# Kernel optimization log

Measured on AMD Instinct MI355X. Metric: run time of the kernel, lower is better.

The kernel has to match this reference:

```python
import jax, jax.numpy as jnp
import numpy as np

B, D, H, L = 16384, 512, 1024, 2


def _lstm_step_zero_state(x, W_ih, W_hh, b_ih, b_hh):
    """One PyTorch-convention LSTM cell step with h0=c0=0.

    Gate order: i, f, g, o. With h0=0 the W_hh matmul contributes nothing,
    but both biases still apply (matches cuDNN/PyTorch math exactly).
    With c0=0 the forget-gate term f*c0 vanishes.
    x: (B, in), W_ih: (4H, in), W_hh: (4H, H), biases: (4H,)
    """
    gates = x @ W_ih.T + (b_ih + b_hh)  # (B, 4H)
    i, f, g, o = jnp.split(gates, 4, axis=-1)
    i = jax.nn.sigmoid(i)
    g = jnp.tanh(g)
    o = jax.nn.sigmoid(o)
    c = i * g  # f * c0 == 0
    h = o * jnp.tanh(c)
    return h


def setup_inputs() -> dict:
    key = jax.random.key(0)
    ks = jax.random.split(key, 12)
    s = 1.0 / np.sqrt(H)  # PyTorch LSTM init scale

    def u(k, shape):
        return jax.random.uniform(k, shape, jnp.float32, -s, s)

    x = jax.random.normal(ks[0], (B, D), jnp.float32)
    return {
        "x": x,
        "W_ih0": u(ks[1], (4 * H, D)),
        "W_hh0": u(ks[2], (4 * H, H)),
        "b_ih0": u(ks[3], (4 * H,)),
        "b_hh0": u(ks[4], (4 * H,)),
        "W_ih1": u(ks[5], (4 * H, H)),
        "W_hh1": u(ks[6], (4 * H, H)),
        "b_ih1": u(ks[7], (4 * H,)),
        "b_hh1": u(ks[8], (4 * H,)),
        "W_dec": u(ks[9], (D, H)),
        "b_dec": u(ks[10], (D,)),
    }


def reference(x, W_ih0, W_hh0, b_ih0, b_hh0, W_ih1, W_hh1, b_ih1, b_hh1, W_dec, b_dec):
    # forward(): x.unsqueeze(1) -> 2-layer LSTM (zero init state, 1 step) -> decoder
    h0 = _lstm_step_zero_state(x, W_ih0, W_hh0, b_ih0, b_hh0)   # (B, H)
    h1 = _lstm_step_zero_state(h0, W_ih1, W_hh1, b_ih1, b_hh1)  # (B, H)
    return h1 @ W_dec.T + b_dec  # (B, D)
```

## Files before the change

kernel.cpp:

```cpp
#include <hip/hip_runtime.h>
#include <stdint.h>


typedef __attribute__((ext_vector_type(8))) __bf16 bf16x8;
typedef __attribute__((ext_vector_type(4))) float f32x4;

#define BM 128
#define BK 64

__device__ __forceinline__ unsigned short f2b(float f) {
    unsigned int x = __builtin_bit_cast(unsigned int, f);
    x = x + 0x7FFFu + ((x >> 16) & 1u);
    return (unsigned short)(x >> 16);
}
__device__ __forceinline__ float sigf(float x) { return 1.0f / (1.0f + __expf(-x)); }
__device__ __forceinline__ float tanh_safe(float x) {
    float a = fabsf(x);
    float e = __expf(-2.0f * a);
    float t = (1.0f - e) / (1.0f + e);
    return x < 0.0f ? -t : t;
}

__device__ __forceinline__ void cvt8(const float* __restrict__ s,
                                     unsigned short* __restrict__ d) {
    f32x4 lo = *reinterpret_cast<const f32x4*>(s);
    f32x4 hi = *reinterpret_cast<const f32x4*>(s + 4);
    __attribute__((ext_vector_type(8))) unsigned short v;
    v[0] = f2b(lo[0]); v[1] = f2b(lo[1]); v[2] = f2b(lo[2]); v[3] = f2b(lo[3]);
    v[4] = f2b(hi[0]); v[5] = f2b(hi[1]); v[6] = f2b(hi[2]); v[7] = f2b(hi[3]);
    *reinterpret_cast<__attribute__((ext_vector_type(8))) unsigned short*>(d) = v;
}

__device__ __forceinline__ void gload16(const unsigned short* g, unsigned short* l) {
    __builtin_amdgcn_global_load_lds(
        (const __attribute__((address_space(1))) void*)g,
        (__attribute__((address_space(3))) void*)l,
        16, 0, 0);
}

__device__ __forceinline__ void pack_one(const float* __restrict__ W,
                                         unsigned short* __restrict__ d,
                                         int K8, int H, int c) {
    int dstRow = c / K8, kc = c - dstRow * K8;
    int G = dstRow / 192, r = dstRow - G * 192;
    int wc = r / 96, rr = r - wc * 96;
    int n = rr >> 4, i = rr & 15;
    int hsub = n / 3, gate = n - hsub * 3;
    int goff = (gate == 0) ? 0 : (gate + 1);
    int hcol = G * 64 + wc * 32 + hsub * 16 + i;
    cvt8(W + ((size_t)(goff * H + hcol) * K8 + kc) * 8, d + (size_t)c * 8);
}

__global__ __launch_bounds__(256) void prepass(
    const float* __restrict__ x,   const float* __restrict__ W0,
    const float* __restrict__ W1,  const float* __restrict__ Wd,
    unsigned short* __restrict__ xb,  unsigned short* __restrict__ wp0,
    unsigned short* __restrict__ wp1, unsigned short* __restrict__ wdecb)
{
    const int tid = threadIdx.x;
    const int b   = blockIdx.x;
    if (b < 2048) {
        int c = b * 256 + tid;
        cvt8(x + (size_t)c * 8, xb + (size_t)c * 8);
        c += 2048 * 256;
        cvt8(x + (size_t)c * 8, xb + (size_t)c * 8);
    } else if (b < 2816) {
        pack_one(W0, wp0, 64, 1024, (b - 2048) * 256 + tid);
    } else if (b < 4352) {
        pack_one(W1, wp1, 128, 1024, (b - 2816) * 256 + tid);
    } else {
        int c = (b - 4352) * 256 + tid;
        cvt8(Wd + (size_t)c * 8, wdecb + (size_t)c * 8);
    }
}

template <int GATED>
__global__ __launch_bounds__(256, 3) void gemm_fused(
    const unsigned short* __restrict__ A,
    const unsigned short* __restrict__ Wp,
    const float* __restrict__ b0,
    const float* __restrict__ b1,
    void* __restrict__ Ov,
    int M, int K, int N, int NBX)
{
    constexpr int NFR   = GATED ? 6 : 4;
    constexpr int BROWS = GATED ? 192 : 128;
    constexpr int WCS   = GATED ? 96 : 64;
    constexpr int ONB   = GATED ? 64 : 128;
    constexpr int NBCH  = BROWS / 32;

    __shared__ __align__(16) unsigned short sA[BM * BK];
    __shared__ __align__(16) unsigned short sB[BROWS * BK];

    const int tid  = threadIdx.x;
    const int lane = tid & 63;
    const int w    = tid >> 6;
    const int wr   = w >> 1, wc = w & 1;
    const int l16  = lane & 15, hi8 = lane >> 4;

    const int cpx  = gridDim.x >> 3;
    const int orig = blockIdx.x;
    const int rid  = (orig & 7) * cpx + (orig >> 3);
    const int bx   = rid % NBX;
    const int by   = rid / NBX;
    const int row0 = by * BM;
    const int n0   = bx * ONB;

    const int r0 = tid >> 3, sl = tid & 7;
    const int ls = sl ^ (r0 & 7);
    const unsigned int strd = 32u * (unsigned)K;
    unsigned int offA = (unsigned)(row0 + r0) * (unsigned)K + ls * 8;
    unsigned int offB = (unsigned)((GATED ? bx * BROWS : n0) + r0)
                        * (unsigned)K + ls * 8;

    f32x4 acc[4][NFR];
#pragma unroll
    for (int m = 0; m < 4; ++m)
#pragma unroll
        for (int n = 0; n < NFR; ++n)
            acc[m][n] = (f32x4){0.f, 0.f, 0.f, 0.f};

    for (int k0 = 0; k0 < K; k0 += BK) {
#pragma unroll
        for (int i = 0; i < 4; ++i)
            gload16(A + offA + i * strd + k0, sA + tid * 8 + i * 2048);
#pragma unroll
        for (int i = 0; i < NBCH; ++i)
            gload16(Wp + offB + i * strd + k0, sB + tid * 8 + i * 2048);
        __syncthreads();

#pragma unroll
        for (int ks = 0; ks < 2; ++ks) {
            bf16x8 av[4], bv[NFR];
#pragma unroll
            for (int m = 0; m < 4; ++m) {
                int row = wr * 64 + m * 16 + l16;
                int ps = (ks * 4 + hi8) ^ (row & 7);
                av[m] = *reinterpret_cast<const bf16x8*>(sA + row * BK + ps * 8);
            }
#pragma unroll
            for (int n = 0; n < NFR; ++n) {
                int row = wc * WCS + n * 16 + l16;
                int ps = (ks * 4 + hi8) ^ (row & 7);
                bv[n] = *reinterpret_cast<const bf16x8*>(sB + row * BK + ps * 8);
            }
#pragma unroll
            for (int m = 0; m < 4; ++m)
#pragma unroll
                for (int n = 0; n < NFR; ++n)
                    acc[m][n] = __builtin_amdgcn_mfma_f32_16x16x32_bf16(
                        av[m], bv[n], acc[m][n], 0, 0, 0);
        }
        __syncthreads();
    }

    if constexpr (GATED) {
        unsigned short* O = (unsigned short*)Ov;
#pragma unroll
        for (int hsub = 0; hsub < 2; ++hsub) {
            const int hcol = n0 + wc * 32 + hsub * 16 + l16;
            const float bi = b0[hcol]         + b1[hcol];
            const float bg = b0[2 * N + hcol] + b1[2 * N + hcol];
            const float bo = b0[3 * N + hcol] + b1[3 * N + hcol];
#pragma unroll
            for (int m = 0; m < 4; ++m) {
                int rbase = row0 + wr * 64 + m * 16 + hi8 * 4;
#pragma unroll
                for (int q = 0; q < 4; ++q) {
                    float iv = sigf(acc[m][hsub * 3 + 0][q] + bi);
                    float gv = tanh_safe(acc[m][hsub * 3 + 1][q] + bg);
                    float ov = sigf(acc[m][hsub * 3 + 2][q] + bo);
                    float h  = ov * tanh_safe(iv * gv);
                    O[(size_t)(rbase + q) * N + hcol] = f2b(h);
                }
            }
        }
    } else {
        float* O = (float*)Ov;
#pragma unroll
        for (int n = 0; n < NFR; ++n) {
            int col = n0 + wc * WCS + n * 16 + l16;
            float bias = b0[col];
#pragma unroll
            for (int m = 0; m < 4; ++m) {
                int rbase = row0 + wr * 64 + m * 16 + hi8 * 4;
#pragma unroll
                for (int q = 0; q < 4; ++q)
                    O[(size_t)(rbase + q) * N + col] = acc[m][n][q] + bias;
            }
        }
    }
}

extern "C" void kernel_launch(void* const* d_in, const int* in_sizes, int n_in,
                              void* d_out, int out_size, void* d_ws, size_t ws_size,
                              hipStream_t stream) {
    constexpr int M = 16384, D = 512, H = 1024;

    const float* x    = (const float*)d_in[0];
    const float* Wih0 = (const float*)d_in[1];
    const float* bih0 = (const float*)d_in[3];
    const float* bhh0 = (const float*)d_in[4];
    const float* Wih1 = (const float*)d_in[5];
    const float* bih1 = (const float*)d_in[7];
    const float* bhh1 = (const float*)d_in[8];
    const float* Wdec = (const float*)d_in[9];
    const float* bdec = (const float*)d_in[10];

    const size_t szH = (size_t)M * H * 2;
    const size_t sw0 = (size_t)3 * H * D * 2;
    const size_t sw1 = (size_t)3 * H * H * 2;

    unsigned short* h0 = (unsigned short*)d_ws;
    unsigned short* h1 = (unsigned short*)((char*)d_ws + szH);
    unsigned short* xb = h1;
    unsigned short* wp0   = (unsigned short*)((char*)d_ws + 2 * szH);
    unsigned short* wp1   = (unsigned short*)((char*)wp0 + sw0);
    unsigned short* wdecb = (unsigned short*)((char*)wp1 + sw1);

    prepass<<<4608, 256, 0, stream>>>(x, Wih0, Wih1, Wdec, xb, wp0, wp1, wdecb);

    gemm_fused<1><<<dim3((H / 64) * (M / BM)), 256, 0, stream>>>(
        xb, wp0, bih0, bhh0, h0, M, D, H, H / 64);
    gemm_fused<1><<<dim3((H / 64) * (M / BM)), 256, 0, stream>>>(
        h0, wp1, bih1, bhh1, h1, M, H, H, H / 64);
    gemm_fused<0><<<dim3((D / 128) * (M / BM)), 256, 0, stream>>>(
        h1, wdecb, bdec, nullptr, (float*)d_out, M, H, D, D / 128);
}
```

Measured before the change: 210.7 us.

## Switch GEMMs to 32x32x16 MFMA tiles and make K a template parameter

Replaces the 16x16x32 bf16 MFMA fragments with 32x32x16 fragments. Each wave now holds 2xNFR 32x32 accumulators instead of 4x(2*NFR) 16x16 ones, which cuts LDS fragment reads per MFMA and raises the math done per instruction. The weight packing order and the gated and plain epilogues are rewritten to match the new accumulator row and column layout. K becomes a compile-time constant so address strides fold. The risk is higher register pressure with f32x16 accumulators and a less coalesced epilogue store pattern.

```diff
diff --git a/kernel.cpp b/kernel.cpp
--- a/kernel.cpp
+++ b/kernel.cpp
@@ -4,6 +4,7 @@
 
 typedef __attribute__((ext_vector_type(8))) __bf16 bf16x8;
 typedef __attribute__((ext_vector_type(4))) float f32x4;
+typedef __attribute__((ext_vector_type(16))) float f32x16;
 
 #define BM 128
 #define BK 64
@@ -43,11 +44,10 @@
                                          int K8, int H, int c) {
     int dstRow = c / K8, kc = c - dstRow * K8;
     int G = dstRow / 192, r = dstRow - G * 192;
-    int wc = r / 96, rr = r - wc * 96;
-    int n = rr >> 4, i = rr & 15;
-    int hsub = n / 3, gate = n - hsub * 3;
+    int wcg = r / 96, rr = r - wcg * 96;
+    int gate = rr >> 5, cc = rr & 31;
     int goff = (gate == 0) ? 0 : (gate + 1);
-    int hcol = G * 64 + wc * 32 + hsub * 16 + i;
+    int hcol = G * 64 + wcg * 32 + cc;
     cvt8(W + ((size_t)(goff * H + hcol) * K8 + kc) * 8, d + (size_t)c * 8);
 }
 
@@ -74,16 +74,16 @@
     }
 }
 
-template <int GATED>
+template <int GATED, int K>
 __global__ __launch_bounds__(256, 3) void gemm_fused(
     const unsigned short* __restrict__ A,
     const unsigned short* __restrict__ Wp,
     const float* __restrict__ b0,
     const float* __restrict__ b1,
     void* __restrict__ Ov,
-    int M, int K, int N, int NBX)
+    int M, int N, int NBX)
 {
-    constexpr int NFR   = GATED ? 6 : 4;
+    constexpr int NFR   = GATED ? 3 : 2;
     constexpr int BROWS = GATED ? 192 : 128;
     constexpr int WCS   = GATED ? 96 : 64;
     constexpr int ONB   = GATED ? 64 : 128;
@@ -96,7 +96,7 @@
     const int lane = tid & 63;
     const int w    = tid >> 6;
     const int wr   = w >> 1, wc = w & 1;
-    const int l16  = lane & 15, hi8 = lane >> 4;
+    const int l32  = lane & 31, hi2 = lane >> 5;
 
     const int cpx  = gridDim.x >> 3;
     const int orig = blockIdx.x;
@@ -108,17 +108,19 @@
 
     const int r0 = tid >> 3, sl = tid & 7;
     const int ls = sl ^ (r0 & 7);
-    const unsigned int strd = 32u * (unsigned)K;
-    unsigned int offA = (unsigned)(row0 + r0) * (unsigned)K + ls * 8;
-    unsigned int offB = (unsigned)((GATED ? bx * BROWS : n0) + r0)
-                        * (unsigned)K + ls * 8;
-
-    f32x4 acc[4][NFR];
-#pragma unroll
-    for (int m = 0; m < 4; ++m)
+    constexpr unsigned int strd = 32u * (unsigned)K;
+    const unsigned int offA = (unsigned)(row0 + r0) * (unsigned)K + ls * 8;
+    const unsigned int offB = (unsigned)((GATED ? bx * BROWS : n0) + r0)
+                              * (unsigned)K + ls * 8;
+
+    f32x16 acc[2][NFR];
+#pragma unroll
+    for (int mf = 0; mf < 2; ++mf)
 #pragma unroll
         for (int n = 0; n < NFR; ++n)
-            acc[m][n] = (f32x4){0.f, 0.f, 0.f, 0.f};
+#pragma unroll
+            for (int q = 0; q < 16; ++q)
+                acc[mf][n][q] = 0.f;
 
     for (int k0 = 0; k0 < K; k0 += BK) {
 #pragma unroll
@@ -130,63 +132,63 @@
         __syncthreads();
 
 #pragma unroll
-        for (int ks = 0; ks < 2; ++ks) {
-            bf16x8 av[4], bv[NFR];
-#pragma unroll
-            for (int m = 0; m < 4; ++m) {
-                int row = wr * 64 + m * 16 + l16;
-                int ps = (ks * 4 + hi8) ^ (row & 7);
-                av[m] = *reinterpret_cast<const bf16x8*>(sA + row * BK + ps * 8);
+        for (int kst = 0; kst < 4; ++kst) {
+            bf16x8 av[2], bv[NFR];
+#pragma unroll
+            for (int mf = 0; mf < 2; ++mf) {
+                int row = wr * 64 + mf * 32 + l32;
+                int ps = (kst * 2 + hi2) ^ (row & 7);
+                av[mf] = *reinterpret_cast<const bf16x8*>(sA + row * BK + ps * 8);
             }
 #pragma unroll
             for (int n = 0; n < NFR; ++n) {
-                int row = wc * WCS + n * 16 + l16;
-                int ps = (ks * 4 + hi8) ^ (row & 7);
+                int row = wc * WCS + n * 32 + l32;
+                int ps = (kst * 2 + hi2) ^ (row & 7);
                 bv[n] = *reinterpret_cast<const bf16x8*>(sB + row * BK + ps * 8);
             }
 #pragma unroll
-            for (int m = 0; m < 4; ++m)
+            for (int mf = 0; mf < 2; ++mf)
 #pragma unroll
                 for (int n = 0; n < NFR; ++n)
-                    acc[m][n] = __builtin_amdgcn_mfma_f32_16x16x32_bf16(
-                        av[m], bv[n], acc[m][n], 0, 0, 0);
+                    acc[mf][n] = __builtin_amdgcn_mfma_f32_32x32x16_bf16(
+                        av[mf], bv[n], acc[mf][n], 0, 0, 0);
         }
         __syncthreads();
     }
 
     if constexpr (GATED) {
         unsigned short* O = (unsigned short*)Ov;
-#pragma unroll
-        for (int hsub = 0; hsub < 2; ++hsub) {
-            const int hcol = n0 + wc * 32 + hsub * 16 + l16;
-            const float bi = b0[hcol]         + b1[hcol];
-            const float bg = b0[2 * N + hcol] + b1[2 * N + hcol];
-            const float bo = b0[3 * N + hcol] + b1[3 * N + hcol];
-#pragma unroll
-            for (int m = 0; m < 4; ++m) {
-                int rbase = row0 + wr * 64 + m * 16 + hi8 * 4;
-#pragma unroll
-                for (int q = 0; q < 4; ++q) {
-                    float iv = sigf(acc[m][hsub * 3 + 0][q] + bi);
-                    float gv = tanh_safe(acc[m][hsub * 3 + 1][q] + bg);
-                    float ov = sigf(acc[m][hsub * 3 + 2][q] + bo);
-                    float h  = ov * tanh_safe(iv * gv);
-                    O[(size_t)(rbase + q) * N + hcol] = f2b(h);
-                }
+        const int hcol = n0 + wc * 32 + l32;
+        const float bi = b0[hcol]         + b1[hcol];
+        const float bg = b0[2 * N + hcol] + b1[2 * N + hcol];
+        const float bo = b0[3 * N + hcol] + b1[3 * N + hcol];
+#pragma unroll
+        for (int mf = 0; mf < 2; ++mf) {
+#pragma unroll
+            for (int reg = 0; reg < 16; ++reg) {
+                int row = row0 + wr * 64 + mf * 32
+                        + (reg & 3) + 8 * (reg >> 2) + 4 * hi2;
+                float iv = sigf(acc[mf][0][reg] + bi);
+                float gv = tanh_safe(acc[mf][1][reg] + bg);
+                float ov = sigf(acc[mf][2][reg] + bo);
+                float h  = ov * tanh_safe(iv * gv);
+                O[(size_t)row * N + hcol] = f2b(h);
             }
         }
     } else {
         float* O = (float*)Ov;
 #pragma unroll
         for (int n = 0; n < NFR; ++n) {
-            int col = n0 + wc * WCS + n * 16 + l16;
+            int col = n0 + wc * WCS + n * 32 + l32;
             float bias = b0[col];
 #pragma unroll
-            for (int m = 0; m < 4; ++m) {
-                int rbase = row0 + wr * 64 + m * 16 + hi8 * 4;
-#pragma unroll
-                for (int q = 0; q < 4; ++q)
-                    O[(size_t)(rbase + q) * N + col] = acc[m][n][q] + bias;
+            for (int mf = 0; mf < 2; ++mf) {
+#pragma unroll
+                for (int reg = 0; reg < 16; ++reg) {
+                    int row = row0 + wr * 64 + mf * 32
+                            + (reg & 3) + 8 * (reg >> 2) + 4 * hi2;
+                    O[(size_t)row * N + col] = acc[mf][n][reg] + bias;
+                }
             }
         }
     }
@@ -220,10 +222,10 @@
 
     prepass<<<4608, 256, 0, stream>>>(x, Wih0, Wih1, Wdec, xb, wp0, wp1, wdecb);
 
-    gemm_fused<1><<<dim3((H / 64) * (M / BM)), 256, 0, stream>>>(
-        xb, wp0, bih0, bhh0, h0, M, D, H, H / 64);
-    gemm_fused<1><<<dim3((H / 64) * (M / BM)), 256, 0, stream>>>(
-        h0, wp1, bih1, bhh1, h1, M, H, H, H / 64);
-    gemm_fused<0><<<dim3((D / 128) * (M / BM)), 256, 0, stream>>>(
-        h1, wdecb, bdec, nullptr, (float*)d_out, M, H, D, D / 128);
-}
+    gemm_fused<1, 512><<<dim3((H / 64) * (M / BM)), 256, 0, stream>>>(
+        xb, wp0, bih0, bhh0, h0, M, H, H / 64);
+    gemm_fused<1, 1024><<<dim3((H / 64) * (M / BM)), 256, 0, stream>>>(
+        h0, wp1, bih1, bhh1, h1, M, H, H / 64);
+    gemm_fused<0, 1024><<<dim3((D / 128) * (M / BM)), 256, 0, stream>>>(
+        h1, wdecb, bdec, nullptr, (float*)d_out, M, D, D / 128);
+}
```

Result: slower. 225.3 us (+6.9%).
